# Kernel tuning notes

Hardware: AMD Instinct MI355X
Metric: run time of the kernel (lower is better)

The kernel has to match this reference:

```python
import jax, jax.numpy as jnp
import numpy as np

B, S, NH, HD = 2, 2048, 32, 128     # batch seqs, tokens per seq, heads, head_dim
H = NH * HD                          # hidden = 4096
BLOCK = 64                           # paged KV-cache block size
NBLK = S // BLOCK                    # blocks per sequence
NUM_BLOCKS = B * NBLK                # total cache blocks


def alibi_slopes(n):
    # n is a power of two: slope_i = 2^(-8*(i+1)/n)
    return np.asarray([2.0 ** (-8.0 * (i + 1) / n) for i in range(n)], dtype=np.float32)


def setup_inputs() -> dict:
    key = jax.random.key(0)
    k1, k2, k3 = jax.random.split(key, 3)
    hidden_states = jax.random.normal(k1, (B * S, H), jnp.float32)
    w_pack = jax.random.normal(k2, (H, 3 * H), jnp.float32) * 0.02
    o_proj_w = jax.random.normal(k3, (H, H), jnp.float32) * 0.02
    k_cache = jnp.zeros((NUM_BLOCKS, BLOCK, NH, HD), jnp.float32)
    v_cache = jnp.zeros((NUM_BLOCKS, BLOCK, NH, HD), jnp.float32)
    block_offsets = jnp.arange(NUM_BLOCKS, dtype=jnp.int32).reshape(B, NBLK)
    return {
        "hidden_states": hidden_states,
        "w_pack": w_pack,
        "o_proj_w": o_proj_w,
        "k_cache": k_cache,
        "v_cache": v_cache,
        "block_offsets": block_offsets,
    }


def reference(hidden_states, w_pack, o_proj_w, k_cache, v_cache, block_offsets):
    # fused QKV projection, chunk(3, -1)
    qkv = hidden_states @ w_pack                      # [B*S, 3H]
    q, k, v = jnp.split(qkv, 3, axis=-1)
    q = q.reshape(B, S, NH, HD)
    k = k.reshape(B, NBLK, BLOCK, NH, HD)
    v = v.reshape(B, NBLK, BLOCK, NH, HD)

    # fill_kv_cache: scatter new K/V into paged cache blocks
    k_cache = k_cache.at[block_offsets].set(k)        # [NUM_BLOCKS, BLOCK, NH, HD]
    v_cache = v_cache.at[block_offsets].set(v)

    # paged read: gather non-contiguous blocks back per sequence
    kg = k_cache[block_offsets].reshape(B, S, NH, HD)
    vg = v_cache[block_offsets].reshape(B, S, NH, HD)

    slopes = jnp.asarray(alibi_slopes(NH))            # [NH]
    scale = 1.0 / jnp.sqrt(jnp.float32(HD))
    scores = jnp.einsum('bqhd,bkhd->bhqk', q, kg) * scale   # [B,NH,S,S]
    pos = jnp.arange(S)
    # ALiBi bias: slope * key_position (row-shift invariant under softmax)
    scores = scores + slopes[None, :, None, None] * pos[None, None, None, :]
    causal = pos[:, None] >= pos[None, :]             # [S,S]
    scores = jnp.where(causal[None, None], scores, jnp.float32(-1e30))
    probs = jax.nn.softmax(scores, axis=-1)
    attn = jnp.einsum('bhqk,bkhd->bqhd', probs, vg).reshape(B * S, H)
    return attn @ o_proj_w
```

## Files before the change

### kernel.cpp

```cpp
#include <hip/hip_runtime.h>
#include <hip/hip_bf16.h>
#include <stdint.h>

typedef __attribute__((ext_vector_type(4))) float f32x4;
typedef __attribute__((ext_vector_type(8))) __bf16 bf16x8;
typedef __attribute__((ext_vector_type(8))) unsigned short u16x8;
typedef __attribute__((ext_vector_type(4))) unsigned short u16x4;
typedef __attribute__((ext_vector_type(2))) unsigned int u32x2;
typedef __attribute__((ext_vector_type(4))) unsigned int u32x4;

#define GLL16(g, l) __builtin_amdgcn_global_load_lds( \
    (const __attribute__((address_space(1))) unsigned int*)(uintptr_t)(g), \
    (__attribute__((address_space(3))) unsigned int*)(uintptr_t)(l), 16, 0, 0)

__device__ __forceinline__ unsigned short bf16u(float f) {
  return __builtin_bit_cast(unsigned short, __float2bfloat16(f));
}

#define PB 2
#define PS 2048
#define PNH 32
#define PHD 128
#define PH 4096
#define P3H 12288

__global__ __launch_bounds__(256)
void cvt_f32_bf16(const float* __restrict__ in, unsigned short* __restrict__ out, int n) {
  int stride = gridDim.x * blockDim.x;
  for (int i = blockIdx.x * blockDim.x + threadIdx.x; i * 8 < n; i += stride) {
    int base = i * 8;
    f32x4 a = *(const f32x4*)(in + base);
    f32x4 b = *(const f32x4*)(in + base + 4);
    u16x8 o;
#pragma unroll
    for (int j = 0; j < 4; ++j) { o[j] = bf16u(a[j]); o[4 + j] = bf16u(b[j]); }
    *(u16x8*)(out + base) = o;
  }
}

__global__ __launch_bounds__(256)
void transpose_cvt(const float* __restrict__ in, unsigned short* __restrict__ out,
                   int K, int N) {
  __shared__ __align__(16) unsigned short tile[64][68];
  int k0 = blockIdx.y * 64, n0 = blockIdx.x * 64;
  int t = threadIdx.x;
  int rr = t >> 4, cc = (t & 15) * 4;
#pragma unroll
  for (int p = 0; p < 4; ++p) {
    int r = rr + p * 16;
    f32x4 v = *(const f32x4*)(in + (size_t)(k0 + r) * N + n0 + cc);
    u16x4 w;
#pragma unroll
    for (int j = 0; j < 4; ++j) w[j] = bf16u(v[j]);
    *(u16x4*)&tile[r][cc] = w;
  }
  __syncthreads();
#pragma unroll
  for (int p = 0; p < 4; ++p) {
    int nl = rr + p * 16;
    u16x4 w;
#pragma unroll
    for (int j = 0; j < 4; ++j) w[j] = tile[cc + j][nl];
    *(u16x4*)(out + (size_t)(n0 + nl) * K + k0 + cc) = w;
  }
}

#define GLLP(TT, P) do { int sb_ = ((TT) & 3) << 15; \
    const unsigned short* s_ = (P) == 0 ? aSrc0 : (P) == 1 ? aSrc1 : (P) == 2 ? bSrc0 : bSrc1; \
    GLL16(s_ + (size_t)(TT) * 32, smem + sb_ + ((P) << 13) + (wave << 10)); } while (0)

#define RD_AV(DST, BUFP, I) DST[I] = *(const bf16x8*)((BUFP) + (((wm << 7) + ((I) << 4) + lr) << 6) + lchunk)
#define RD_BV(DST, BUFP, J) DST[J] = *(const bf16x8*)((BUFP) + 16384 + (((wn << 6) + ((J) << 4) + lr) << 6) + lchunk)

#define SGB __builtin_amdgcn_sched_group_barrier

#define TILE(TC, AC, AN, DOSTAGE, DOREAD, VM, DOBAR) do { \
    char* nA_ = smem + ((((TC) + 1) & 3) << 15); \
    __builtin_amdgcn_s_setprio(1); \
    _Pragma("unroll") \
    for (int g = 0; g < 4; ++g) { \
      if (DOREAD) { RD_AV(AN, nA_, 2 * g); RD_AV(AN, nA_, 2 * g + 1); } \
      if (DOSTAGE) GLLP((TC) + 3, g); \
      _Pragma("unroll") \
      for (int i = 2 * g; i < 2 * g + 2; ++i) \
        _Pragma("unroll") \
        for (int j = 0; j < 4; ++j) \
          acc[i][j] = __builtin_amdgcn_mfma_f32_16x16x32_bf16(AC[i], bvv[j], acc[i][j], 0, 0, 0); \
      SGB(0x100, 2, 0); SGB(0x020, 1, 0); SGB(0x008, 8, 0); \
    } \
    if (DOREAD) { RD_BV(bvv, nA_, 0); RD_BV(bvv, nA_, 1); RD_BV(bvv, nA_, 2); RD_BV(bvv, nA_, 3); } \
    __builtin_amdgcn_s_setprio(0); \
    if ((VM) == 4)      asm volatile("s_waitcnt vmcnt(4)" ::: "memory"); \
    else if ((VM) == 0) asm volatile("s_waitcnt vmcnt(0)" ::: "memory"); \
    if (DOBAR) __builtin_amdgcn_s_barrier(); \
  } while (0)

template<int OUTF32>
__global__ __launch_bounds__(512, 2)
void gemm256(const unsigned short* __restrict__ A, const unsigned short* __restrict__ Bt,
             void* __restrict__ Cv, int M, int N, int K) {
  __shared__ __align__(16) char smem[131072];
  const int tid = threadIdx.x;
  const int wave = tid >> 6, lane = tid & 63;
  const int lr = lane & 15, lg = lane >> 4;
  const int wm = wave >> 2, wn = wave & 3;
  const int lchunk = (lg ^ ((lr >> 1) & 3)) << 4;
  const int nbn = N >> 8;
  const int nwg = (M >> 8) * nbn;
  int bid = blockIdx.x;
  int qq = nwg >> 3;
  int wg = (bid & 7) * qq + (bid >> 3);
  int bm = wg / nbn, bn = wg % nbn;
  const size_t arow = (size_t)bm << 8;
  const size_t brow = (size_t)bn << 8;

  const int srow = (wave << 4) + (lane >> 2);
  const int scol = ((lane & 3) ^ ((lane >> 3) & 3)) << 3;
  const unsigned short* aSrc0 = A  + (arow + srow) * K + scol;
  const unsigned short* aSrc1 = A  + (arow + 128 + srow) * K + scol;
  const unsigned short* bSrc0 = Bt + (brow + srow) * K + scol;
  const unsigned short* bSrc1 = Bt + (brow + 128 + srow) * K + scol;

  f32x4 acc[8][4] = {};

#pragma unroll
  for (int p = 0; p < 4; ++p) GLLP(0, p);
#pragma unroll
  for (int p = 0; p < 4; ++p) GLLP(1, p);
#pragma unroll
  for (int p = 0; p < 4; ++p) GLLP(2, p);
  asm volatile("s_waitcnt vmcnt(4)" ::: "memory");
  __builtin_amdgcn_s_barrier();

  bf16x8 avA[8], avB[8], bvv[4];
  {
    char* b0 = smem;
#pragma unroll
    for (int i = 0; i < 8; ++i) RD_AV(avA, b0, i);
#pragma unroll
    for (int j = 0; j < 4; ++j) RD_BV(bvv, b0, j);
  }

  for (int p = 0; p < 62; ++p) {
    int t = 2 * p;
    TILE(t,     avA, avB, 1, 1, 4, 1);
    TILE(t + 1, avB, avA, 1, 1, 4, 1);
  }
  TILE(124, avA, avB, 1, 1, 4, 1);
  TILE(125, avB, avA, 0, 1, 0, 1);
  TILE(126, avA, avB, 0, 1, -1, 0);
  TILE(127, avB, avA, 0, 0, -1, 0);

  int crow = (bm << 8) + (wm << 7) + (lg << 2);
  int ccol = (bn << 8) + (wn << 6) + lr;
#pragma unroll
  for (int i = 0; i < 8; ++i)
#pragma unroll
    for (int j = 0; j < 4; ++j)
#pragma unroll
      for (int r = 0; r < 4; ++r) {
        size_t off = (size_t)(crow + (i << 4) + r) * N + ccol + (j << 4);
        if (OUTF32) ((float*)Cv)[off] = acc[i][j][r];
        else        ((unsigned short*)Cv)[off] = bf16u(acc[i][j][r]);
      }
}

__global__ __launch_bounds__(256, 2)
void attn_kernel(const unsigned short* __restrict__ qkv, unsigned short* __restrict__ out) {
  __shared__ __align__(16) unsigned short Ks[2][64 * 128];
  __shared__ __align__(16) unsigned short Vt[128 * 64];
  __shared__ __align__(16) unsigned short Ps[4][32 * 88];
  int tid = threadIdx.x, wave = tid >> 6, lane = tid & 63;
  int lr = lane & 15, lg = lane >> 4;
  int idx = blockIdx.x;
  int qt = 15 - (idx & 15);
  int h = (idx >> 4) & 31, b = idx >> 9;
  size_t rb = (size_t)b * PS;
  int qcol = h << 7, kcol = PH + (h << 7), vcol = 2 * PH + (h << 7);
  int q0 = (qt << 7) + (wave << 5);

  bf16x8 aq[2][4];
#pragma unroll
  for (int qs = 0; qs < 2; ++qs)
#pragma unroll
    for (int f = 0; f < 4; ++f)
      aq[qs][f] = *(const bf16x8*)(qkv + (rb + q0 + (qs << 4) + lr) * P3H + qcol + (f << 5) + (lg << 3));

  float m_run[2][4], l_run[2][4];
#pragma unroll
  for (int qs = 0; qs < 2; ++qs)
#pragma unroll
    for (int r = 0; r < 4; ++r) { m_run[qs][r] = -1e30f; l_run[qs][r] = 0.f; }
  f32x4 acc_o[2][8] = {};

  float slope2 = __builtin_amdgcn_exp2f(-(float)(h + 1) * 0.25f) * 1.44269504f;
  const float scale2 = 0.08838834764831845f * 1.44269504f;

  char* KsB = (char*)Ks;
  char* VtB = (char*)Vt;
  const int kk0 = (tid & 15) << 2, d0 = (tid >> 4) << 3;

  {
    size_t krow = rb;
#pragma unroll
    for (int i = 0; i < 4; ++i) {
      int pf = (wave << 12) | (i << 10) | (lane << 4);
      int row = pf >> 8;
      int lch = ((pf >> 4) & 15) ^ (row & 7);
      GLL16(qkv + (krow + row) * P3H + kcol + (lch << 3), KsB + (wave << 12) + (i << 10));
    }
  }
  u32x4 vr0 = *(const u32x4*)(qkv + (rb + kk0 + 0) * P3H + vcol + d0);
  u32x4 vr1 = *(const u32x4*)(qkv + (rb + kk0 + 1) * P3H + vcol + d0);
  u32x4 vr2 = *(const u32x4*)(qkv + (rb + kk0 + 2) * P3H + vcol + d0);
  u32x4 vr3 = *(const u32x4*)(qkv + (rb + kk0 + 3) * P3H + vcol + d0);

  const int tmax = 2 * qt + 1;
  for (int t = 0; t <= tmax; ++t) {
    int cur = t & 1;
    char* KsCur = KsB + (cur << 14);
    char* KsNxt = KsB + ((cur ^ 1) << 14);
    bool more = (t < tmax);

    u32x4 nv0 = {}, nv1 = {}, nv2 = {}, nv3 = {};
    if (more) {
      size_t krow = rb + ((size_t)(t + 1) << 6);
#pragma unroll
      for (int i = 0; i < 4; ++i) {
        int pf = (wave << 12) | (i << 10) | (lane << 4);
        int row = pf >> 8;
        int lch = ((pf >> 4) & 15) ^ (row & 7);
        GLL16(qkv + (krow + row) * P3H + kcol + (lch << 3), KsNxt + (wave << 12) + (i << 10));
      }
      nv0 = *(const u32x4*)(qkv + (krow + kk0 + 0) * P3H + vcol + d0);
      nv1 = *(const u32x4*)(qkv + (krow + kk0 + 1) * P3H + vcol + d0);
      nv2 = *(const u32x4*)(qkv + (krow + kk0 + 2) * P3H + vcol + d0);
      nv3 = *(const u32x4*)(qkv + (krow + kk0 + 3) * P3H + vcol + d0);
    }

    if (more) asm volatile("s_waitcnt vmcnt(8)" ::: "memory");
    else      asm volatile("s_waitcnt vmcnt(0)" ::: "memory");

    {
      const unsigned short* e0 = (const unsigned short*)&vr0;
      const unsigned short* e1 = (const unsigned short*)&vr1;
      const unsigned short* e2 = (const unsigned short*)&vr2;
      const unsigned short* e3 = (const unsigned short*)&vr3;
#pragma unroll
      for (int j = 0; j < 8; ++j) {
        int d = d0 + j;
        u32x2 w;
        w.x = (unsigned int)e0[j] | ((unsigned int)e1[j] << 16);
        w.y = (unsigned int)e2[j] | ((unsigned int)e3[j] << 16);
        int byteoff = ((d << 7) + (kk0 << 1)) ^ ((d & 7) << 4);
        *(u32x2*)(VtB + byteoff) = w;
      }
    }
    asm volatile("s_waitcnt lgkmcnt(0)" ::: "memory");
    __builtin_amdgcn_s_barrier();

    f32x4 sc[2][4];
    __builtin_amdgcn_s_setprio(1);
#pragma unroll
    for (int f = 0; f < 4; ++f) {
      f32x4 c0 = {}, c1 = {};
#pragma unroll
      for (int ks = 0; ks < 4; ++ks) {
        int kkr = (f << 4) + lr;
        int ch = (lg + (ks << 2)) ^ (kkr & 7);
        bf16x8 bk = *(const bf16x8*)(KsCur + (kkr << 8) + (ch << 4));
        c0 = __builtin_amdgcn_mfma_f32_16x16x32_bf16(aq[0][ks], bk, c0, 0, 0, 0);
        c1 = __builtin_amdgcn_mfma_f32_16x16x32_bf16(aq[1][ks], bk, c1, 0, 0, 0);
      }
      sc[0][f] = c0; sc[1][f] = c1;
    }
    __builtin_amdgcn_s_setprio(0);

    int kvb = t << 6;
    bool needmask = (kvb + 63 > q0);
#pragma unroll
    for (int qs = 0; qs < 2; ++qs) {
      float vals[4][4];
#pragma unroll
      for (int f = 0; f < 4; ++f) {
        int kv = kvb + (f << 4) + lr;
        float bias = slope2 * (float)kv;
#pragma unroll
        for (int r = 0; r < 4; ++r) {
          float v = sc[qs][f][r] * scale2 + bias;
          if (needmask && kv > q0 + (qs << 4) + (lg << 2) + r) v = -1e30f;
          vals[r][f] = v;
        }
      }
      float alpha[4];
#pragma unroll
      for (int r = 0; r < 4; ++r) {
        float mr = fmaxf(fmaxf(vals[r][0], vals[r][1]), fmaxf(vals[r][2], vals[r][3]));
#pragma unroll
        for (int d2 = 1; d2 < 16; d2 <<= 1) mr = fmaxf(mr, __shfl_xor(mr, d2, 16));
        float mnew = fmaxf(m_run[qs][r], mr);
        alpha[r] = __builtin_amdgcn_exp2f(m_run[qs][r] - mnew);
        m_run[qs][r] = mnew;
      }
#pragma unroll
      for (int r = 0; r < 4; ++r) {
        float s = 0.f;
#pragma unroll
        for (int f = 0; f < 4; ++f) {
          float p = __builtin_amdgcn_exp2f(vals[r][f] - m_run[qs][r]);
          s += p;
          Ps[wave][((qs << 4) + (lg << 2) + r) * 88 + (f << 4) + lr] = bf16u(p);
        }
        l_run[qs][r] = l_run[qs][r] * alpha[r] + s;
      }
#pragma unroll
      for (int d = 0; d < 8; ++d) {
        f32x4 a4 = acc_o[qs][d];
#pragma unroll
        for (int r = 0; r < 4; ++r) a4[r] *= alpha[r];
        acc_o[qs][d] = a4;
      }
    }

    bf16x8 pa[2][2];
#pragma unroll
    for (int qs = 0; qs < 2; ++qs)
#pragma unroll
      for (int ks = 0; ks < 2; ++ks)
        pa[qs][ks] = *(const bf16x8*)((char*)&Ps[wave][0] + ((qs << 4) + lr) * 176 + (ks << 6) + (lg << 4));
    __builtin_amdgcn_s_setprio(1);
#pragma unroll
    for (int d = 0; d < 8; ++d) {
#pragma unroll
      for (int ks = 0; ks < 2; ++ks) {
        int dr = (d << 4) + lr;
        int ch = (lg + (ks << 2)) ^ (dr & 7);
        bf16x8 bv = *(const bf16x8*)(VtB + (dr << 7) + (ch << 4));
        acc_o[0][d] = __builtin_amdgcn_mfma_f32_16x16x32_bf16(pa[0][ks], bv, acc_o[0][d], 0, 0, 0);
        acc_o[1][d] = __builtin_amdgcn_mfma_f32_16x16x32_bf16(pa[1][ks], bv, acc_o[1][d], 0, 0, 0);
      }
    }
    __builtin_amdgcn_s_setprio(0);
    __builtin_amdgcn_s_barrier();

    if (more) { vr0 = nv0; vr1 = nv1; vr2 = nv2; vr3 = nv3; }
  }

#pragma unroll
  for (int qs = 0; qs < 2; ++qs) {
    float rinv[4];
#pragma unroll
    for (int r = 0; r < 4; ++r) {
      float s = l_run[qs][r];
#pragma unroll
      for (int d2 = 1; d2 < 16; d2 <<= 1) s += __shfl_xor(s, d2, 16);
      rinv[r] = 1.f / s;
    }
#pragma unroll
    for (int d = 0; d < 8; ++d)
#pragma unroll
      for (int r = 0; r < 4; ++r) {
        float o = acc_o[qs][d][r] * rinv[r];
        out[(rb + q0 + (qs << 4) + (lg << 2) + r) * PH + (h << 7) + (d << 4) + lr] = bf16u(o);
      }
  }
}

extern "C" void kernel_launch(void* const* d_in, const int* in_sizes, int n_in,
                              void* d_out, int out_size, void* d_ws, size_t ws_size,
                              hipStream_t stream) {
  const float* hidden = (const float*)d_in[0];
  const float* w_pack = (const float*)d_in[1];
  const float* o_proj = (const float*)d_in[2];

  char* ws = (char*)d_ws;
  unsigned short* wpackT = (unsigned short*)(ws);
  unsigned short* qkv    = (unsigned short*)(ws + 100663296);
  unsigned short* oprojT = (unsigned short*)(ws + 201326592);
  unsigned short* hbf    = (unsigned short*)(ws + 234881024);
  unsigned short* attnb  = hbf;

  int M = PB * PS;

  cvt_f32_bf16<<<2048, 256, 0, stream>>>(hidden, hbf, M * PH);
  transpose_cvt<<<dim3(P3H / 64, PH / 64), 256, 0, stream>>>(w_pack, wpackT, PH, P3H);
  transpose_cvt<<<dim3(PH / 64, PH / 64), 256, 0, stream>>>(o_proj, oprojT, PH, PH);
  gemm256<0><<<(M / 256) * (P3H / 256), 512, 0, stream>>>(hbf, wpackT, qkv, M, P3H, PH);
  attn_kernel<<<PB * PNH * (PS / 128), 256, 0, stream>>>(qkv, attnb);
  gemm256<1><<<(M / 256) * (PH / 256), 512, 0, stream>>>(attnb, oprojT, d_out, M, PH, PH);
}
```

Before: 850.5 us.

## Split attention softmax per subtile, interleave with PV MFMAs, lazy rescale

Moves the attention softmax into a per-16-row macro. Rescaling of the running max and accumulator is skipped unless some row's max grows by more than 8 (log2 units), checked wave-wide. The second subtile's softmax now sits before the first subtile's PV MFMAs, and sched_group_barrier hints interleave those MFMAs with VALU and LDS work to overlap exp math with matrix ops. The lazy rescale cuts exp and multiply work on the accumulators. Its risk is a larger fp32 dynamic range in the accumulators and possible extra register pressure.

```diff
diff --git a/kernel.cpp b/kernel.cpp
--- a/kernel.cpp
+++ b/kernel.cpp
@@ -165,6 +165,57 @@
       }
 }
 
+#define ATTN_SOFTMAX(QS) do { \
+    float vals[4][4]; \
+    _Pragma("unroll") \
+    for (int f = 0; f < 4; ++f) { \
+      int kv = kvb + (f << 4) + lr; \
+      float bias = slope2 * (float)kv; \
+      _Pragma("unroll") \
+      for (int r = 0; r < 4; ++r) { \
+        float v = sc[QS][f][r] * scale2 + bias; \
+        if (needmask && kv > q0 + ((QS) << 4) + (lg << 2) + r) v = -1e30f; \
+        vals[r][f] = v; \
+      } \
+    } \
+    float mnew[4]; int keep = 1; \
+    _Pragma("unroll") \
+    for (int r = 0; r < 4; ++r) { \
+      float mr = fmaxf(fmaxf(vals[r][0], vals[r][1]), fmaxf(vals[r][2], vals[r][3])); \
+      _Pragma("unroll") \
+      for (int d2 = 1; d2 < 16; d2 <<= 1) mr = fmaxf(mr, __shfl_xor(mr, d2, 16)); \
+      mnew[r] = fmaxf(m_run[QS][r], mr); \
+      keep = keep & (mnew[r] - m_run[QS][r] <= 8.f ? 1 : 0); \
+    } \
+    if (!__all(keep)) { \
+      float alpha[4]; \
+      _Pragma("unroll") \
+      for (int r = 0; r < 4; ++r) { \
+        alpha[r] = __builtin_amdgcn_exp2f(m_run[QS][r] - mnew[r]); \
+        m_run[QS][r] = mnew[r]; \
+        l_run[QS][r] *= alpha[r]; \
+      } \
+      _Pragma("unroll") \
+      for (int d = 0; d < 8; ++d) { \
+        f32x4 a4 = acc_o[QS][d]; \
+        _Pragma("unroll") \
+        for (int r = 0; r < 4; ++r) a4[r] *= alpha[r]; \
+        acc_o[QS][d] = a4; \
+      } \
+    } \
+    _Pragma("unroll") \
+    for (int r = 0; r < 4; ++r) { \
+      float s = 0.f; \
+      _Pragma("unroll") \
+      for (int f = 0; f < 4; ++f) { \
+        float p = __builtin_amdgcn_exp2f(vals[r][f] - m_run[QS][r]); \
+        s += p; \
+        Ps[wave][(((QS) << 4) + (lg << 2) + r) * 88 + (f << 4) + lr] = bf16u(p); \
+      } \
+      l_run[QS][r] += s; \
+    } \
+  } while (0)
+
 __global__ __launch_bounds__(256, 2)
 void attn_kernel(const unsigned short* __restrict__ qkv, unsigned short* __restrict__ out) {
   __shared__ __align__(16) unsigned short Ks[2][64 * 128];
@@ -278,56 +329,14 @@
 
     int kvb = t << 6;
     bool needmask = (kvb + 63 > q0);
-#pragma unroll
-    for (int qs = 0; qs < 2; ++qs) {
-      float vals[4][4];
-#pragma unroll
-      for (int f = 0; f < 4; ++f) {
-        int kv = kvb + (f << 4) + lr;
-        float bias = slope2 * (float)kv;
-#pragma unroll
-        for (int r = 0; r < 4; ++r) {
-          float v = sc[qs][f][r] * scale2 + bias;
-          if (needmask && kv > q0 + (qs << 4) + (lg << 2) + r) v = -1e30f;
-          vals[r][f] = v;
-        }
-      }
-      float alpha[4];
-#pragma unroll
-      for (int r = 0; r < 4; ++r) {
-        float mr = fmaxf(fmaxf(vals[r][0], vals[r][1]), fmaxf(vals[r][2], vals[r][3]));
-#pragma unroll
-        for (int d2 = 1; d2 < 16; d2 <<= 1) mr = fmaxf(mr, __shfl_xor(mr, d2, 16));
-        float mnew = fmaxf(m_run[qs][r], mr);
-        alpha[r] = __builtin_amdgcn_exp2f(m_run[qs][r] - mnew);
-        m_run[qs][r] = mnew;
-      }
-#pragma unroll
-      for (int r = 0; r < 4; ++r) {
-        float s = 0.f;
-#pragma unroll
-        for (int f = 0; f < 4; ++f) {
-          float p = __builtin_amdgcn_exp2f(vals[r][f] - m_run[qs][r]);
-          s += p;
-          Ps[wave][((qs << 4) + (lg << 2) + r) * 88 + (f << 4) + lr] = bf16u(p);
-        }
-        l_run[qs][r] = l_run[qs][r] * alpha[r] + s;
-      }
-#pragma unroll
-      for (int d = 0; d < 8; ++d) {
-        f32x4 a4 = acc_o[qs][d];
-#pragma unroll
-        for (int r = 0; r < 4; ++r) a4[r] *= alpha[r];
-        acc_o[qs][d] = a4;
-      }
-    }
-
-    bf16x8 pa[2][2];
-#pragma unroll
-    for (int qs = 0; qs < 2; ++qs)
-#pragma unroll
-      for (int ks = 0; ks < 2; ++ks)
-        pa[qs][ks] = *(const bf16x8*)((char*)&Ps[wave][0] + ((qs << 4) + lr) * 176 + (ks << 6) + (lg << 4));
+
+    ATTN_SOFTMAX(0);
+    bf16x8 pa0[2];
+#pragma unroll
+    for (int ks = 0; ks < 2; ++ks)
+      pa0[ks] = *(const bf16x8*)((char*)&Ps[wave][0] + lr * 176 + (ks << 6) + (lg << 4));
+
+    ATTN_SOFTMAX(1);
     __builtin_amdgcn_s_setprio(1);
 #pragma unroll
     for (int d = 0; d < 8; ++d) {
@@ -336,8 +345,25 @@
         int dr = (d << 4) + lr;
         int ch = (lg + (ks << 2)) ^ (dr & 7);
         bf16x8 bv = *(const bf16x8*)(VtB + (dr << 7) + (ch << 4));
-        acc_o[0][d] = __builtin_amdgcn_mfma_f32_16x16x32_bf16(pa[0][ks], bv, acc_o[0][d], 0, 0, 0);
-        acc_o[1][d] = __builtin_amdgcn_mfma_f32_16x16x32_bf16(pa[1][ks], bv, acc_o[1][d], 0, 0, 0);
+        acc_o[0][d] = __builtin_amdgcn_mfma_f32_16x16x32_bf16(pa0[ks], bv, acc_o[0][d], 0, 0, 0);
+      }
+      SGB(0x100, 2, 0); SGB(0x008, 2, 0); SGB(0x002, 24, 0);
+    }
+    __builtin_amdgcn_s_setprio(0);
+
+    bf16x8 pa1[2];
+#pragma unroll
+    for (int ks = 0; ks < 2; ++ks)
+      pa1[ks] = *(const bf16x8*)((char*)&Ps[wave][0] + (16 + lr) * 176 + (ks << 6) + (lg << 4));
+    __builtin_amdgcn_s_setprio(1);
+#pragma unroll
+    for (int d = 0; d < 8; ++d) {
+#pragma unroll
+      for (int ks = 0; ks < 2; ++ks) {
+        int dr = (d << 4) + lr;
+        int ch = (lg + (ks << 2)) ^ (dr & 7);
+        bf16x8 bv = *(const bf16x8*)(VtB + (dr << 7) + (ch << 4));
+        acc_o[1][d] = __builtin_amdgcn_mfma_f32_16x16x32_bf16(pa1[ks], bv, acc_o[1][d], 0, 0, 0);
       }
     }
     __builtin_amdgcn_s_setprio(0);
```

After: 864.6 us. No clear change (+1.7%).

## Halve attention tile sizes to 64-row Q tiles and 32-key KV tiles

Applied to the files above, without the earlier changes.

The attention kernel now uses 64 query rows per block (16 per wave) and 32-key KV tiles instead of 128 and 64. The launch grid doubles and launch bounds rise to allow 4 blocks per CU. The V-transpose LDS layout gets a new XOR swizzle suited to 32-wide rows. The aim is more parallelism and occupancy, at the cost of less K/V reuse per load and twice as many barriers per key range.

```diff
diff --git a/kernel.cpp b/kernel.cpp
--- a/kernel.cpp
+++ b/kernel.cpp
@@ -6,7 +6,6 @@
 typedef __attribute__((ext_vector_type(8))) __bf16 bf16x8;
 typedef __attribute__((ext_vector_type(8))) unsigned short u16x8;
 typedef __attribute__((ext_vector_type(4))) unsigned short u16x4;
-typedef __attribute__((ext_vector_type(2))) unsigned int u32x2;
 typedef __attribute__((ext_vector_type(4))) unsigned int u32x4;
 
 #define GLL16(g, l) __builtin_amdgcn_global_load_lds( \
@@ -165,205 +164,178 @@
       }
 }
 
-__global__ __launch_bounds__(256, 2)
+__global__ __launch_bounds__(256, 4)
 void attn_kernel(const unsigned short* __restrict__ qkv, unsigned short* __restrict__ out) {
-  __shared__ __align__(16) unsigned short Ks[2][64 * 128];
-  __shared__ __align__(16) unsigned short Vt[128 * 64];
-  __shared__ __align__(16) unsigned short Ps[4][32 * 88];
+  __shared__ __align__(16) unsigned short Ks[2][32 * 128];
+  __shared__ __align__(16) unsigned short Vt[128 * 32];
+  __shared__ __align__(16) unsigned short Ps[4][16 * 40];
   int tid = threadIdx.x, wave = tid >> 6, lane = tid & 63;
   int lr = lane & 15, lg = lane >> 4;
   int idx = blockIdx.x;
-  int qt = 15 - (idx & 15);
-  int h = (idx >> 4) & 31, b = idx >> 9;
+  int qt = 31 - (idx & 31);
+  int h = (idx >> 5) & 31, b = idx >> 10;
   size_t rb = (size_t)b * PS;
   int qcol = h << 7, kcol = PH + (h << 7), vcol = 2 * PH + (h << 7);
-  int q0 = (qt << 7) + (wave << 5);
-
-  bf16x8 aq[2][4];
-#pragma unroll
-  for (int qs = 0; qs < 2; ++qs)
-#pragma unroll
-    for (int f = 0; f < 4; ++f)
-      aq[qs][f] = *(const bf16x8*)(qkv + (rb + q0 + (qs << 4) + lr) * P3H + qcol + (f << 5) + (lg << 3));
-
-  float m_run[2][4], l_run[2][4];
-#pragma unroll
-  for (int qs = 0; qs < 2; ++qs)
-#pragma unroll
-    for (int r = 0; r < 4; ++r) { m_run[qs][r] = -1e30f; l_run[qs][r] = 0.f; }
-  f32x4 acc_o[2][8] = {};
+  int q0 = (qt << 6) + (wave << 4);
+
+  bf16x8 aq[4];
+#pragma unroll
+  for (int f = 0; f < 4; ++f)
+    aq[f] = *(const bf16x8*)(qkv + (rb + q0 + lr) * P3H + qcol + (f << 5) + (lg << 3));
+
+  float m_run[4] = {-1e30f, -1e30f, -1e30f, -1e30f};
+  float l_run[4] = {0.f, 0.f, 0.f, 0.f};
+  f32x4 acc_o[8] = {};
 
   float slope2 = __builtin_amdgcn_exp2f(-(float)(h + 1) * 0.25f) * 1.44269504f;
   const float scale2 = 0.08838834764831845f * 1.44269504f;
 
   char* KsB = (char*)Ks;
   char* VtB = (char*)Vt;
-  const int kk0 = (tid & 15) << 2, d0 = (tid >> 4) << 3;
+  const int kk0 = (tid & 15) << 1;
+  const int d0 = (tid >> 4) << 3;
 
   {
     size_t krow = rb;
 #pragma unroll
-    for (int i = 0; i < 4; ++i) {
-      int pf = (wave << 12) | (i << 10) | (lane << 4);
+    for (int i = 0; i < 2; ++i) {
+      int pf = (wave << 11) | (i << 10) | (lane << 4);
       int row = pf >> 8;
       int lch = ((pf >> 4) & 15) ^ (row & 7);
-      GLL16(qkv + (krow + row) * P3H + kcol + (lch << 3), KsB + (wave << 12) + (i << 10));
+      GLL16(qkv + (krow + row) * P3H + kcol + (lch << 3), KsB + (wave << 11) + (i << 10));
     }
   }
   u32x4 vr0 = *(const u32x4*)(qkv + (rb + kk0 + 0) * P3H + vcol + d0);
   u32x4 vr1 = *(const u32x4*)(qkv + (rb + kk0 + 1) * P3H + vcol + d0);
-  u32x4 vr2 = *(const u32x4*)(qkv + (rb + kk0 + 2) * P3H + vcol + d0);
-  u32x4 vr3 = *(const u32x4*)(qkv + (rb + kk0 + 3) * P3H + vcol + d0);
 
   const int tmax = 2 * qt + 1;
   for (int t = 0; t <= tmax; ++t) {
     int cur = t & 1;
-    char* KsCur = KsB + (cur << 14);
-    char* KsNxt = KsB + ((cur ^ 1) << 14);
+    char* KsCur = KsB + (cur << 13);
+    char* KsNxt = KsB + ((cur ^ 1) << 13);
     bool more = (t < tmax);
 
-    u32x4 nv0 = {}, nv1 = {}, nv2 = {}, nv3 = {};
+    u32x4 nv0 = {}, nv1 = {};
     if (more) {
-      size_t krow = rb + ((size_t)(t + 1) << 6);
-#pragma unroll
-      for (int i = 0; i < 4; ++i) {
-        int pf = (wave << 12) | (i << 10) | (lane << 4);
+      size_t krow = rb + ((size_t)(t + 1) << 5);
+#pragma unroll
+      for (int i = 0; i < 2; ++i) {
+        int pf = (wave << 11) | (i << 10) | (lane << 4);
         int row = pf >> 8;
         int lch = ((pf >> 4) & 15) ^ (row & 7);
-        GLL16(qkv + (krow + row) * P3H + kcol + (lch << 3), KsNxt + (wave << 12) + (i << 10));
+        GLL16(qkv + (krow + row) * P3H + kcol + (lch << 3), KsNxt + (wave << 11) + (i << 10));
       }
       nv0 = *(const u32x4*)(qkv + (krow + kk0 + 0) * P3H + vcol + d0);
       nv1 = *(const u32x4*)(qkv + (krow + kk0 + 1) * P3H + vcol + d0);
-      nv2 = *(const u32x4*)(qkv + (krow + kk0 + 2) * P3H + vcol + d0);
-      nv3 = *(const u32x4*)(qkv + (krow + kk0 + 3) * P3H + vcol + d0);
-    }
-
-    if (more) asm volatile("s_waitcnt vmcnt(8)" ::: "memory");
+    }
+
+    if (more) asm volatile("s_waitcnt vmcnt(4)" ::: "memory");
     else      asm volatile("s_waitcnt vmcnt(0)" ::: "memory");
 
     {
       const unsigned short* e0 = (const unsigned short*)&vr0;
       const unsigned short* e1 = (const unsigned short*)&vr1;
-      const unsigned short* e2 = (const unsigned short*)&vr2;
-      const unsigned short* e3 = (const unsigned short*)&vr3;
 #pragma unroll
       for (int j = 0; j < 8; ++j) {
         int d = d0 + j;
-        u32x2 w;
-        w.x = (unsigned int)e0[j] | ((unsigned int)e1[j] << 16);
-        w.y = (unsigned int)e2[j] | ((unsigned int)e3[j] << 16);
-        int byteoff = ((d << 7) + (kk0 << 1)) ^ ((d & 7) << 4);
-        *(u32x2*)(VtB + byteoff) = w;
+        unsigned int w = (unsigned int)e0[j] | ((unsigned int)e1[j] << 16);
+        int c = (kk0 >> 3) ^ (((d >> 1) ^ (d >> 3)) & 3);
+        int byteoff = (d << 6) + (c << 4) + ((kk0 << 1) & 15);
+        *(unsigned int*)(VtB + byteoff) = w;
       }
     }
     asm volatile("s_waitcnt lgkmcnt(0)" ::: "memory");
     __builtin_amdgcn_s_barrier();
 
-    f32x4 sc[2][4];
+    f32x4 sc[2];
     __builtin_amdgcn_s_setprio(1);
 #pragma unroll
-    for (int f = 0; f < 4; ++f) {
-      f32x4 c0 = {}, c1 = {};
+    for (int f = 0; f < 2; ++f) {
+      f32x4 c = {};
 #pragma unroll
       for (int ks = 0; ks < 4; ++ks) {
         int kkr = (f << 4) + lr;
         int ch = (lg + (ks << 2)) ^ (kkr & 7);
         bf16x8 bk = *(const bf16x8*)(KsCur + (kkr << 8) + (ch << 4));
-        c0 = __builtin_amdgcn_mfma_f32_16x16x32_bf16(aq[0][ks], bk, c0, 0, 0, 0);
-        c1 = __builtin_amdgcn_mfma_f32_16x16x32_bf16(aq[1][ks], bk, c1, 0, 0, 0);
-      }
-      sc[0][f] = c0; sc[1][f] = c1;
+        c = __builtin_amdgcn_mfma_f32_16x16x32_bf16(aq[ks], bk, c, 0, 0, 0);
+      }
+      sc[f] = c;
     }
     __builtin_amdgcn_s_setprio(0);
 
-    int kvb = t << 6;
-    bool needmask = (kvb + 63 > q0);
-#pragma unroll
-    for (int qs = 0; qs < 2; ++qs) {
-      float vals[4][4];
-#pragma unroll
-      for (int f = 0; f < 4; ++f) {
-        int kv = kvb + (f << 4) + lr;
-        float bias = slope2 * (float)kv;
-#pragma unroll
-        for (int r = 0; r < 4; ++r) {
-          float v = sc[qs][f][r] * scale2 + bias;
-          if (needmask && kv > q0 + (qs << 4) + (lg << 2) + r) v = -1e30f;
-          vals[r][f] = v;
-        }
-      }
-      float alpha[4];
+    int kvb = t << 5;
+    bool needmask = (kvb + 31 > q0);
+    float vals[4][2];
+#pragma unroll
+    for (int f = 0; f < 2; ++f) {
+      int kv = kvb + (f << 4) + lr;
+      float bias = slope2 * (float)kv;
 #pragma unroll
       for (int r = 0; r < 4; ++r) {
-        float mr = fmaxf(fmaxf(vals[r][0], vals[r][1]), fmaxf(vals[r][2], vals[r][3]));
-#pragma unroll
-        for (int d2 = 1; d2 < 16; d2 <<= 1) mr = fmaxf(mr, __shfl_xor(mr, d2, 16));
-        float mnew = fmaxf(m_run[qs][r], mr);
-        alpha[r] = __builtin_amdgcn_exp2f(m_run[qs][r] - mnew);
-        m_run[qs][r] = mnew;
-      }
-#pragma unroll
-      for (int r = 0; r < 4; ++r) {
-        float s = 0.f;
-#pragma unroll
-        for (int f = 0; f < 4; ++f) {
-          float p = __builtin_amdgcn_exp2f(vals[r][f] - m_run[qs][r]);
-          s += p;
-          Ps[wave][((qs << 4) + (lg << 2) + r) * 88 + (f << 4) + lr] = bf16u(p);
-        }
-        l_run[qs][r] = l_run[qs][r] * alpha[r] + s;
-      }
-#pragma unroll
-      for (int d = 0; d < 8; ++d) {
-        f32x4 a4 = acc_o[qs][d];
-#pragma unroll
-        for (int r = 0; r < 4; ++r) a4[r] *= alpha[r];
-        acc_o[qs][d] = a4;
-      }
-    }
-
-    bf16x8 pa[2][2];
-#pragma unroll
-    for (int qs = 0; qs < 2; ++qs)
-#pragma unroll
-      for (int ks = 0; ks < 2; ++ks)
-        pa[qs][ks] = *(const bf16x8*)((char*)&Ps[wave][0] + ((qs << 4) + lr) * 176 + (ks << 6) + (lg << 4));
+        float v = sc[f][r] * scale2 + bias;
+        if (needmask && kv > q0 + (lg << 2) + r) v = -1e30f;
+        vals[r][f] = v;
+      }
+    }
+    float alpha[4];
+#pragma unroll
+    for (int r = 0; r < 4; ++r) {
+      float mr = fmaxf(vals[r][0], vals[r][1]);
+#pragma unroll
+      for (int d2 = 1; d2 < 16; d2 <<= 1) mr = fmaxf(mr, __shfl_xor(mr, d2, 16));
+      float mnew = fmaxf(m_run[r], mr);
+      alpha[r] = __builtin_amdgcn_exp2f(m_run[r] - mnew);
+      m_run[r] = mnew;
+    }
+#pragma unroll
+    for (int r = 0; r < 4; ++r) {
+      float s = 0.f;
+#pragma unroll
+      for (int f = 0; f < 2; ++f) {
+        float p = __builtin_amdgcn_exp2f(vals[r][f] - m_run[r]);
+        s += p;
+        Ps[wave][((lg << 2) + r) * 40 + (f << 4) + lr] = bf16u(p);
+      }
+      l_run[r] = l_run[r] * alpha[r] + s;
+    }
+#pragma unroll
+    for (int d = 0; d < 8; ++d) {
+      f32x4 a4 = acc_o[d];
+#pragma unroll
+      for (int r = 0; r < 4; ++r) a4[r] *= alpha[r];
+      acc_o[d] = a4;
+    }
+
+    bf16x8 pa = *(const bf16x8*)((char*)&Ps[wave][0] + lr * 80 + (lg << 4));
     __builtin_amdgcn_s_setprio(1);
 #pragma unroll
     for (int d = 0; d < 8; ++d) {
-#pragma unroll
-      for (int ks = 0; ks < 2; ++ks) {
-        int dr = (d << 4) + lr;
-        int ch = (lg + (ks << 2)) ^ (dr & 7);
-        bf16x8 bv = *(const bf16x8*)(VtB + (dr << 7) + (ch << 4));
-        acc_o[0][d] = __builtin_amdgcn_mfma_f32_16x16x32_bf16(pa[0][ks], bv, acc_o[0][d], 0, 0, 0);
-        acc_o[1][d] = __builtin_amdgcn_mfma_f32_16x16x32_bf16(pa[1][ks], bv, acc_o[1][d], 0, 0, 0);
-      }
+      int dr = (d << 4) + lr;
+      int ch = lg ^ (((dr >> 1) ^ (dr >> 3)) & 3);
+      bf16x8 bv = *(const bf16x8*)(VtB + (dr << 6) + (ch << 4));
+      acc_o[d] = __builtin_amdgcn_mfma_f32_16x16x32_bf16(pa, bv, acc_o[d], 0, 0, 0);
     }
     __builtin_amdgcn_s_setprio(0);
     __builtin_amdgcn_s_barrier();
 
-    if (more) { vr0 = nv0; vr1 = nv1; vr2 = nv2; vr3 = nv3; }
-  }
-
-#pragma unroll
-  for (int qs = 0; qs < 2; ++qs) {
-    float rinv[4];
+    if (more) { vr0 = nv0; vr1 = nv1; }
+  }
+
+  float rinv[4];
+#pragma unroll
+  for (int r = 0; r < 4; ++r) {
+    float s = l_run[r];
+#pragma unroll
+    for (int d2 = 1; d2 < 16; d2 <<= 1) s += __shfl_xor(s, d2, 16);
+    rinv[r] = 1.f / s;
+  }
+#pragma unroll
+  for (int d = 0; d < 8; ++d)
 #pragma unroll
     for (int r = 0; r < 4; ++r) {
-      float s = l_run[qs][r];
-#pragma unroll
-      for (int d2 = 1; d2 < 16; d2 <<= 1) s += __shfl_xor(s, d2, 16);
-      rinv[r] = 1.f / s;
-    }
-#pragma unroll
-    for (int d = 0; d < 8; ++d)
-#pragma unroll
-      for (int r = 0; r < 4; ++r) {
-        float o = acc_o[qs][d][r] * rinv[r];
-        out[(rb + q0 + (qs << 4) + (lg << 2) + r) * PH + (h << 7) + (d << 4) + lr] = bf16u(o);
-      }
-  }
+      float o = acc_o[d][r] * rinv[r];
+      out[(rb + q0 + (lg << 2) + r) * PH + (h << 7) + (d << 4) + lr] = bf16u(o);
+    }
 }
 
 extern "C" void kernel_launch(void* const* d_in, const int* in_sizes, int n_in,
@@ -386,6 +358,6 @@
   transpose_cvt<<<dim3(P3H / 64, PH / 64), 256, 0, stream>>>(w_pack, wpackT, PH, P3H);
   transpose_cvt<<<dim3(PH / 64, PH / 64), 256, 0, stream>>>(o_proj, oprojT, PH, PH);
   gemm256<0><<<(M / 256) * (P3H / 256), 512, 0, stream>>>(hbf, wpackT, qkv, M, P3H, PH);
-  attn_kernel<<<PB * PNH * (PS / 128), 256, 0, stream>>>(qkv, attnb);
+  attn_kernel<<<PB * PNH * (PS / 64), 256, 0, stream>>>(qkv, attnb);
   gemm256<1><<<(M / 256) * (PH / 256), 512, 0, stream>>>(attnb, oprojT, d_out, M, PH, PH);
 }
```

Result: slower. 895.9 us (+5.3%).
